# Kernel optimization log

Hardware: AMD Instinct MI355X
Metric: run time of the kernel (lower is better)

Reference implementation:

```python
import jax, jax.numpy as jnp
import numpy as np

N_NODES = 50000
N_EDGES = 800000
ATOM_DIM = 32
EDGE_DIM = 16
HIDDEN = 64
NUM_STEPS = 3
NUM_GRAPHS = 256
OUT_DIM = 1


def setup_inputs() -> dict:
    key = jax.random.key(0)
    ks = jax.random.split(key, 20)
    s = 0.05
    inp = {
        "x": jax.random.normal(ks[0], (N_NODES, ATOM_DIM), dtype=jnp.float32),
        "edge_index": jax.random.randint(ks[1], (2, N_EDGES), 0, N_NODES),
        "edge_attr": jax.random.normal(ks[2], (N_EDGES, EDGE_DIM), dtype=jnp.float32),
        "batch": jnp.sort(jax.random.randint(ks[3], (N_NODES,), 0, NUM_GRAPHS)),
        # atom embedding
        "W_embed": jax.random.normal(ks[4], (ATOM_DIM, HIDDEN)) * s,
        "b_embed": jnp.zeros((HIDDEN,)),
        # message MLP: Linear(2H+E, H) -> ReLU -> Linear(H, H)
        "W_m1": jax.random.normal(ks[5], (2 * HIDDEN + EDGE_DIM, HIDDEN)) * s,
        "b_m1": jnp.zeros((HIDDEN,)),
        "W_m2": jax.random.normal(ks[6], (HIDDEN, HIDDEN)) * s,
        "b_m2": jnp.zeros((HIDDEN,)),
        # GRUCell (torch layout: [3H, in] stacked r,z,n)
        "W_ih": jax.random.normal(ks[7], (3 * HIDDEN, HIDDEN)) * s,
        "b_ih": jnp.zeros((3 * HIDDEN,)),
        "W_hh": jax.random.normal(ks[8], (3 * HIDDEN, HIDDEN)) * s,
        "b_hh": jnp.zeros((3 * HIDDEN,)),
        # head: Linear(2H, H) -> ReLU -> Linear(H, out)
        "W_h1": jax.random.normal(ks[9], (2 * HIDDEN, HIDDEN)) * s,
        "b_h1": jnp.zeros((HIDDEN,)),
        "W_h2": jax.random.normal(ks[10], (HIDDEN, OUT_DIM)) * s,
        "b_h2": jnp.zeros((OUT_DIM,)),
    }
    return inp


def _gru_cell(inp, h, W_ih, b_ih, W_hh, b_hh):
    gi = inp @ W_ih.T + b_ih   # [N, 3H]
    gh = h @ W_hh.T + b_hh     # [N, 3H]
    i_r, i_z, i_n = jnp.split(gi, 3, axis=-1)
    h_r, h_z, h_n = jnp.split(gh, 3, axis=-1)
    r = jax.nn.sigmoid(i_r + h_r)
    z = jax.nn.sigmoid(i_z + h_z)
    n = jnp.tanh(i_n + r * h_n)
    return (1.0 - z) * n + z * h


def reference(x, edge_index, edge_attr, batch,
              W_embed, b_embed, W_m1, b_m1, W_m2, b_m2,
              W_ih, b_ih, W_hh, b_hh, W_h1, b_h1, W_h2, b_h2):
    h = x @ W_embed + b_embed                       # [N, H]
    src, dst = edge_index[0], edge_index[1]         # PyG: x_j = x[src], x_i = x[dst]
    for _ in range(NUM_STEPS):                      # tied weights
        m = jnp.concatenate([h[src], h[dst], edge_attr], axis=-1)  # [E, 2H+ED]
        m = jax.nn.relu(m @ W_m1 + b_m1) @ W_m2 + b_m2             # [E, H]
        agg = jax.ops.segment_sum(m, dst, num_segments=N_NODES)    # scatter-add
        h = _gru_cell(agg, h, W_ih, b_ih, W_hh, b_hh)
    g_sum = jax.ops.segment_sum(h, batch, num_segments=NUM_GRAPHS)  # [G, H]
    cnt = jax.ops.segment_sum(jnp.ones((N_NODES,), h.dtype), batch,
                              num_segments=NUM_GRAPHS)
    g_mean = g_sum / jnp.maximum(cnt, 1.0)[:, None]
    g = jnp.concatenate([g_sum, g_mean], axis=-1)   # [G, 2H]
    return jax.nn.relu(g @ W_h1 + b_h1) @ W_h2 + b_h2  # [G, out]
```

## Files before the change

kernel.cpp:

```cpp
#include <hip/hip_runtime.h>
#include <math.h>

#define NN 50000
#define NE 800000
#define AD 32
#define ED 16
#define HD 64
#define NG 256
#define NTILES (NE / 16)
#define EGRID 1280
#define EGRID_FB 1024
#define TPX (NTILES / 8)
#define GGRID 768
#define GTILES (NN / 16)
#define PGRID 782

typedef short bf16x8 __attribute__((ext_vector_type(8)));
typedef float f32x4  __attribute__((ext_vector_type(4)));
union U4B { uint4 u; bf16x8 v; };

__device__ __forceinline__ float blo(unsigned u){ return __uint_as_float(u << 16); }
__device__ __forceinline__ float bhi(unsigned u){ return __uint_as_float(u & 0xffff0000u); }
__device__ __forceinline__ unsigned short f2bf(float f){
  unsigned u = __float_as_uint(f);
  u += 0x7fffu + ((u >> 16) & 1u);
  return (unsigned short)(u >> 16);
}
__device__ __forceinline__ unsigned packbf2(float a, float b){
  return (unsigned)f2bf(a) | ((unsigned)f2bf(b) << 16);
}
__device__ __forceinline__ bf16x8 ldfrag_g(const unsigned* p){
  U4B x; x.u = *(const uint4*)p; return x.v;
}
__device__ __forceinline__ unsigned srp1(unsigned a, unsigned b, unsigned c){
  float lo = fmaxf(blo(a) + blo(b) + blo(c), 0.f);
  float hi = fmaxf(bhi(a) + bhi(b) + bhi(c), 0.f);
  return packbf2(lo, hi);
}
__device__ __forceinline__ bf16x8 srp4(uint4 a, uint4 b, uint4 c){
  U4B r;
  r.u.x = srp1(a.x, b.x, c.x);
  r.u.y = srp1(a.y, b.y, c.y);
  r.u.z = srp1(a.z, b.z, c.z);
  r.u.w = srp1(a.w, b.w, c.w);
  return r.v;
}

__global__ __launch_bounds__(256) void k_prep(const float* __restrict__ W1,
                                              const float* __restrict__ W2,
                                              const float* __restrict__ Wih,
                                              const float* __restrict__ Whh,
                                              const float* __restrict__ b1,
                                              unsigned short* __restrict__ W1Tp,
                                              unsigned short* __restrict__ W2Tp,
                                              unsigned short* __restrict__ Wgru,
                                              unsigned short* __restrict__ W1cTp)
{
  int idx = blockIdx.x * 256 + threadIdx.x;
  if (idx < 64 * 168){
    int n = idx / 168, k = idx % 168;
    W1Tp[idx] = (k < 144) ? f2bf(W1[k * 64 + n]) : (unsigned short)0;
    return;
  }
  idx -= 64 * 168;
  if (idx < 64 * 72){
    int n = idx / 72, k = idx % 72;
    W2Tp[idx] = (k < 64) ? f2bf(W2[k * 64 + n]) : (unsigned short)0;
    return;
  }
  idx -= 64 * 72;
  if (idx < 384 * 64){
    int j = idx & 7;
    int g = (idx >> 3) % 384;
    int blk = idx >> 3; blk /= 384;
    int q = blk & 3, ks = blk >> 2;
    int k = ks * 32 + q * 8 + j;
    float v = (g < 192) ? Wih[g * 64 + k] : Whh[(g - 192) * 64 + k];
    Wgru[idx] = f2bf(v);
    return;
  }
  idx -= 384 * 64;
  if (idx < 64 * 32){
    int n = idx / 32, k = idx % 32;
    float v = (k < 16) ? W1[(128 + k) * 64 + n] : (k == 16 ? b1[n] : 0.f);
    W1cTp[idx] = f2bf(v);
  }
}

__global__ __launch_bounds__(256) void k_hist(const int* __restrict__ eidx, int* __restrict__ deg)
{
  int e = blockIdx.x * 256 + threadIdx.x;
  if (e < NE) atomicAdd(&deg[eidx[NE + e]], 1);
}

__global__ __launch_bounds__(1024) void k_scan1(const int* __restrict__ deg,
                                                int* __restrict__ cur,
                                                int* __restrict__ bsum)
{
  __shared__ int s[1024];
  const int t = threadIdx.x;
  const int idx = blockIdx.x * 1024 + t;
  int v = (idx < NN) ? deg[idx] : 0;
  s[t] = v;
  __syncthreads();
  for (int d = 1; d < 1024; d <<= 1){
    int y = (t >= d) ? s[t - d] : 0;
    __syncthreads();
    s[t] += y;
    __syncthreads();
  }
  if (idx < NN) cur[idx] = s[t] - v;
  if (t == 1023) bsum[blockIdx.x] = s[1023];
}

__global__ __launch_bounds__(64) void k_scan2(const int* __restrict__ bsum,
                                              int* __restrict__ bpre)
{
  const int t = threadIdx.x;
  const int nb = (NN + 1023) / 1024;
  int v = (t < nb) ? bsum[t] : 0;
  int orig = v;
  #pragma unroll
  for (int off = 1; off < 64; off <<= 1){
    int u = __shfl_up(v, off);
    if (t >= off) v += u;
  }
  if (t < nb) bpre[t] = v - orig;
}

__global__ __launch_bounds__(1024) void k_scan3(int* __restrict__ cur,
                                                const int* __restrict__ bpre)
{
  const int idx = blockIdx.x * 1024 + threadIdx.x;
  if (idx < NN) cur[idx] += bpre[blockIdx.x];
}

__global__ __launch_bounds__(256) void k_scatter(const int* __restrict__ eidx,
                                                 const float* __restrict__ eattr,
                                                 int* __restrict__ cur,
                                                 int* __restrict__ src_s,
                                                 int* __restrict__ dst_s,
                                                 unsigned* __restrict__ eattr_bf)
{
  int e = blockIdx.x * 256 + threadIdx.x;
  if (e >= NE) return;
  int d = eidx[NE + e];
  int p = atomicAdd(&cur[d], 1);
  src_s[p] = eidx[e];
  dst_s[p] = d;
  const float* ea = eattr + (size_t)e * 16;
  float4 v0 = *(const float4*)(ea);
  float4 v1 = *(const float4*)(ea + 4);
  float4 v2 = *(const float4*)(ea + 8);
  float4 v3 = *(const float4*)(ea + 12);
  uint4 o0, o1;
  o0.x = packbf2(v0.x, v0.y); o0.y = packbf2(v0.z, v0.w);
  o0.z = packbf2(v1.x, v1.y); o0.w = packbf2(v1.z, v1.w);
  o1.x = packbf2(v2.x, v2.y); o1.y = packbf2(v2.z, v2.w);
  o1.z = packbf2(v3.x, v3.y); o1.w = packbf2(v3.z, v3.w);
  *(uint4*)(eattr_bf + (size_t)p * 8)     = o0;
  *(uint4*)(eattr_bf + (size_t)p * 8 + 4) = o1;
}

__global__ __launch_bounds__(256) void k_eprep(const unsigned* __restrict__ eattr_bf,
                                               const unsigned* __restrict__ W1cTp32,
                                               unsigned* __restrict__ E1)
{
  const int t = threadIdx.x, lane = t & 63, wv = t >> 6;
  const int m = lane & 15, q = lane >> 4;
  bf16x8 wf[4];
  #pragma unroll
  for (int tl = 0; tl < 4; ++tl)
    wf[tl] = ldfrag_g(W1cTp32 + (tl * 16 + m) * 16 + q * 4);

  for (int wt = blockIdx.x * 4 + wv; wt < NTILES; wt += 1024 * 4){
    const int base = wt * 16;
    U4B x;
    if (q < 2)      x.u = *(const uint4*)(eattr_bf + (size_t)(base + m) * 8 + q * 4);
    else if (q == 2) x.u = make_uint4(0x3F80u, 0, 0, 0);
    else             x.u = make_uint4(0, 0, 0, 0);
    bf16x8 a = x.v;
    f32x4 c[4];
    #pragma unroll
    for (int tl = 0; tl < 4; ++tl) c[tl] = f32x4{0.f,0.f,0.f,0.f};
    #pragma unroll
    for (int tl = 0; tl < 4; ++tl)
      c[tl] = __builtin_amdgcn_mfma_f32_16x16x32_bf16(a, wf[tl], c[tl], 0, 0, 0);
    #pragma unroll
    for (int tl = 0; tl < 4; ++tl){
      #pragma unroll
      for (int rr = 0; rr < 4; ++rr){
        float v = c[tl][rr];
        float pp = __shfl_xor(v, 1);
        if (!(m & 1))
          E1[(size_t)(base + q * 4 + rr) * 32 + (tl * 16 + m) / 2] = packbf2(v, pp);
      }
    }
  }
}

__global__ __launch_bounds__(256, 4) void k_pre(const unsigned* __restrict__ h_bf,
                                                const unsigned short* __restrict__ W1Tp,
                                                unsigned* __restrict__ C12)
{
  const int t = threadIdx.x, lane = t & 63, wv = t >> 6;
  const int m = lane & 15, q = lane >> 4;
  bf16x8 wa[4][2], wb[4][2];
  #pragma unroll
  for (int tl = 0; tl < 4; ++tl)
    #pragma unroll
    for (int ks = 0; ks < 2; ++ks){
      wa[tl][ks] = ldfrag_g((const unsigned*)(W1Tp + (tl * 16 + m) * 168 + ks * 32 + q * 8));
      wb[tl][ks] = ldfrag_g((const unsigned*)(W1Tp + (tl * 16 + m) * 168 + 64 + ks * 32 + q * 8));
    }
  for (int wt = blockIdx.x * 4 + wv; wt < GTILES; wt += PGRID * 4){
    const int n0 = wt * 16;
    bf16x8 aH[2];
    #pragma unroll
    for (int ks = 0; ks < 2; ++ks)
      aH[ks] = ldfrag_g(h_bf + (size_t)(n0 + m) * 32 + ks * 16 + q * 4);
    f32x4 ca[4], cb[4];
    #pragma unroll
    for (int tl = 0; tl < 4; ++tl){ ca[tl] = f32x4{0.f,0.f,0.f,0.f}; cb[tl] = ca[tl]; }
    #pragma unroll
    for (int ks = 0; ks < 2; ++ks)
      #pragma unroll
      for (int tl = 0; tl < 4; ++tl){
        ca[tl] = __builtin_amdgcn_mfma_f32_16x16x32_bf16(aH[ks], wa[tl][ks], ca[tl], 0, 0, 0);
        cb[tl] = __builtin_amdgcn_mfma_f32_16x16x32_bf16(aH[ks], wb[tl][ks], cb[tl], 0, 0, 0);
      }
    #pragma unroll
    for (int tl = 0; tl < 4; ++tl){
      #pragma unroll
      for (int rr = 0; rr < 4; ++rr){
        const int node = n0 + q * 4 + rr;
        float va = ca[tl][rr], vb = cb[tl][rr];
        float pa = __shfl_xor(va, 1), pb = __shfl_xor(vb, 1);
        if (!(m & 1)){
          C12[(size_t)node * 64 + (tl * 16 + m) / 2]      = packbf2(va, pa);
          C12[(size_t)node * 64 + 32 + (tl * 16 + m) / 2] = packbf2(vb, pb);
        }
      }
    }
  }
}

__global__ __launch_bounds__(256) void k_embed(const float* __restrict__ x,
                                               const float* __restrict__ We,
                                               const float* __restrict__ be,
                                               float* __restrict__ h,
                                               unsigned* __restrict__ h_bf)
{
  const int t = threadIdx.x;
  const int j = t & 63, nd = t >> 6;
  const int node = blockIdx.x * 4 + nd;
  const float* xr = x + (size_t)node * AD;
  float acc = be[j];
  #pragma unroll 8
  for (int k = 0; k < AD; ++k)
    acc += xr[k] * We[k * HD + j];
  h[(size_t)node * HD + j] = acc;
  float p = __shfl_down(acc, 1);
  if (!(j & 1)) h_bf[(size_t)node * 32 + (j >> 1)] = packbf2(acc, p);
}

__global__ __launch_bounds__(256, 4) void k_edge(const unsigned* __restrict__ C12,
                                                 const unsigned* __restrict__ E1,
                                                 const int* __restrict__ src_s,
                                                 const int* __restrict__ dst_s,
                                                 const unsigned* __restrict__ W2Tp32,
                                                 const float* __restrict__ b2,
                                                 float* __restrict__ agg)
{
  const int t = threadIdx.x;
  const int lane = t & 63, wv = t >> 6;
  const int m = lane & 15, q = lane >> 4;

  bf16x8 w2f[4][2];
  #pragma unroll
  for (int tl = 0; tl < 4; ++tl)
    #pragma unroll
    for (int ks = 0; ks < 2; ++ks)
      w2f[tl][ks] = ldfrag_g(W2Tp32 + (tl * 16 + m) * 36 + ks * 16 + q * 4);

  float b2v[4];
  #pragma unroll
  for (int tl = 0; tl < 4; ++tl) b2v[tl] = b2[tl * 16 + m];

  const int xcd = blockIdx.x & 7, bi = blockIdx.x >> 3;
  const int wend = (xcd + 1) * TPX;
  const int wstep = (EGRID / 8) * 4;
  int wt = xcd * TPX + bi * 4 + wv;

  int scur = src_s[wt * 16 + m];
  int dcur = dst_s[wt * 16 + m];

  while (wt < wend){
    const int wn = wt + wstep;
    const bool hasn = (wn < wend);
    int sn = 0, dn = 0;
    if (hasn){ sn = src_s[wn * 16 + m]; dn = dst_s[wn * 16 + m]; }

    const unsigned* c1p = C12 + (size_t)scur * 64;
    const unsigned* c2p = C12 + (size_t)dcur * 64 + 32;
    const unsigned* e1p = E1 + (size_t)(wt * 16 + m) * 32;
    uint4 c1a = *(const uint4*)(c1p + q * 4);
    uint4 c1b = *(const uint4*)(c1p + 16 + q * 4);
    uint4 c2a = *(const uint4*)(c2p + q * 4);
    uint4 c2b = *(const uint4*)(c2p + 16 + q * 4);
    uint4 e1a = *(const uint4*)(e1p + q * 4);
    uint4 e1b = *(const uint4*)(e1p + 16 + q * 4);

    bf16x8 af0 = srp4(c1a, c2a, e1a);
    bf16x8 af1 = srp4(c1b, c2b, e1b);

    f32x4 o0 = {0.f,0.f,0.f,0.f}, o1 = o0, o2 = o0, o3 = o0;
    o0 = __builtin_amdgcn_mfma_f32_16x16x32_bf16(af0, w2f[0][0], o0, 0, 0, 0);
    o1 = __builtin_amdgcn_mfma_f32_16x16x32_bf16(af0, w2f[1][0], o1, 0, 0, 0);
    o2 = __builtin_amdgcn_mfma_f32_16x16x32_bf16(af0, w2f[2][0], o2, 0, 0, 0);
    o3 = __builtin_amdgcn_mfma_f32_16x16x32_bf16(af0, w2f[3][0], o3, 0, 0, 0);
    o0 = __builtin_amdgcn_mfma_f32_16x16x32_bf16(af1, w2f[0][1], o0, 0, 0, 0);
    o1 = __builtin_amdgcn_mfma_f32_16x16x32_bf16(af1, w2f[1][1], o1, 0, 0, 0);
    o2 = __builtin_amdgcn_mfma_f32_16x16x32_bf16(af1, w2f[2][1], o2, 0, 0, 0);
    o3 = __builtin_amdgcn_mfma_f32_16x16x32_bf16(af1, w2f[3][1], o3, 0, 0, 0);

    int prev = __shfl_up(dcur, 1);
    bool isStart = (m == 0) || (dcur != prev);
    unsigned long long bal = __ballot(isStart);
    unsigned bs = (unsigned)bal & 0xFFFFu;
    int nr = __popc(bs);
    unsigned rem = bs & (bs - 1);
    int lo = 0;
    for (int r = 0; r < nr; ++r){
      int hi = rem ? (__ffs(rem) - 1) : 16;
      rem &= rem - 1;
      float s0 = 0.f, s1 = 0.f, s2 = 0.f, s3 = 0.f;
      #pragma unroll
      for (int rr = 0; rr < 4; ++rr){
        int row = q * 4 + rr;
        bool in = (row >= lo) && (row < hi);
        s0 += in ? o0[rr] : 0.f;
        s1 += in ? o1[rr] : 0.f;
        s2 += in ? o2[rr] : 0.f;
        s3 += in ? o3[rr] : 0.f;
      }
      s0 += __shfl_xor(s0, 16); s0 += __shfl_xor(s0, 32);
      s1 += __shfl_xor(s1, 16); s1 += __shfl_xor(s1, 32);
      s2 += __shfl_xor(s2, 16); s2 += __shfl_xor(s2, 32);
      s3 += __shfl_xor(s3, 16); s3 += __shfl_xor(s3, 32);
      int d = __shfl(dcur, lo);
      float cntf = (float)(hi - lo);
      if (q == 0){
        float v0 = s0 + cntf * b2v[0];
        float v1 = s1 + cntf * b2v[1];
        float v2 = s2 + cntf * b2v[2];
        float v3 = s3 + cntf * b2v[3];
        float* dp = &agg[(size_t)d * HD + m];
        if (r == 0 || r == nr - 1){
          atomicAdd(dp +  0, v0); atomicAdd(dp + 16, v1);
          atomicAdd(dp + 32, v2); atomicAdd(dp + 48, v3);
        } else {
          dp[ 0] = v0; dp[16] = v1; dp[32] = v2; dp[48] = v3;
        }
      }
      lo = hi;
    }

    wt = wn; scur = sn; dcur = dn;
  }
}

__global__ __launch_bounds__(256, 3) void k_edge_fb(const unsigned* __restrict__ h_bf,
                                                    const int* __restrict__ src_s,
                                                    const int* __restrict__ dst_s,
                                                    const unsigned* __restrict__ eattr_bf,
                                                    const unsigned short* __restrict__ W1Tp,
                                                    const float* __restrict__ b1,
                                                    const unsigned* __restrict__ W2Tp32,
                                                    const float* __restrict__ b2,
                                                    float* __restrict__ agg)
{
  __shared__ __align__(16) unsigned short sW1T[64 * 168];
  __shared__ __align__(16) unsigned short sHid[4][16 * 72];

  const int t = threadIdx.x;
  {
    const uint4* srcp = (const uint4*)W1Tp;
    uint4* dstp = (uint4*)sW1T;
    for (int i = t; i < 64 * 168 * 2 / 16; i += 256) dstp[i] = srcp[i];
  }
  __syncthreads();

  const int lane = t & 63, wv = t >> 6;
  const int m = lane & 15, q = lane >> 4;

  bf16x8 w2f[4][2];
  #pragma unroll
  for (int tl = 0; tl < 4; ++tl)
    #pragma unroll
    for (int ks = 0; ks < 2; ++ks)
      w2f[tl][ks] = ldfrag_g(W2Tp32 + (tl * 16 + m) * 36 + ks * 16 + q * 4);

  float b1v[4], b2v[4];
  #pragma unroll
  for (int tl = 0; tl < 4; ++tl){ b1v[tl] = b1[tl * 16 + m]; b2v[tl] = b2[tl * 16 + m]; }

  unsigned short* sHidW = sHid[wv];

  const int xcd = blockIdx.x & 7, bi = blockIdx.x >> 3;
  const int wend = (xcd + 1) * TPX;
  const int wstep = (EGRID_FB / 8) * 4;
  int wt = xcd * TPX + bi * 4 + wv;

  int scur = src_s[wt * 16 + m];
  int dcur = dst_s[wt * 16 + m];
  bf16x8 afc[5];
  {
    const unsigned* hs = h_bf + (size_t)scur * 32;
    const unsigned* hd = h_bf + (size_t)dcur * 32;
    afc[0] = ldfrag_g(hs + q * 4);
    afc[1] = ldfrag_g(hs + 16 + q * 4);
    afc[2] = ldfrag_g(hd + q * 4);
    afc[3] = ldfrag_g(hd + 16 + q * 4);
    if (q < 2) afc[4] = ldfrag_g(eattr_bf + (size_t)(wt * 16 + m) * 8 + q * 4);
    else { U4B x; x.u = make_uint4(0,0,0,0); afc[4] = x.v; }
  }

  while (wt < wend){
    const int wn = wt + wstep;
    const bool hasn = (wn < wend);
    int sn = 0, dn = 0;
    if (hasn){ sn = src_s[wn * 16 + m]; dn = dst_s[wn * 16 + m]; }

    f32x4 a0 = {0.f,0.f,0.f,0.f}, a1 = a0, a2 = a0, a3 = a0;
    #pragma unroll
    for (int ks = 0; ks < 5; ++ks){
      bf16x8 bb0 = *(const bf16x8*)&sW1T[( 0 + m) * 168 + ks * 32 + q * 8];
      bf16x8 bb1 = *(const bf16x8*)&sW1T[(16 + m) * 168 + ks * 32 + q * 8];
      bf16x8 bb2 = *(const bf16x8*)&sW1T[(32 + m) * 168 + ks * 32 + q * 8];
      bf16x8 bb3 = *(const bf16x8*)&sW1T[(48 + m) * 168 + ks * 32 + q * 8];
      a0 = __builtin_amdgcn_mfma_f32_16x16x32_bf16(afc[ks], bb0, a0, 0, 0, 0);
      a1 = __builtin_amdgcn_mfma_f32_16x16x32_bf16(afc[ks], bb1, a1, 0, 0, 0);
      a2 = __builtin_amdgcn_mfma_f32_16x16x32_bf16(afc[ks], bb2, a2, 0, 0, 0);
      a3 = __builtin_amdgcn_mfma_f32_16x16x32_bf16(afc[ks], bb3, a3, 0, 0, 0);
    }
    {
      f32x4 accs[4] = {a0, a1, a2, a3};
      #pragma unroll
      for (int tl = 0; tl < 4; ++tl)
        #pragma unroll
        for (int r = 0; r < 4; ++r)
          sHidW[(q * 4 + r) * 72 + tl * 16 + m] = f2bf(fmaxf(accs[tl][r] + b1v[tl], 0.f));
    }

    bf16x8 afn[5];
    if (hasn){
      const unsigned* hs = h_bf + (size_t)sn * 32;
      const unsigned* hd = h_bf + (size_t)dn * 32;
      afn[0] = ldfrag_g(hs + q * 4);
      afn[1] = ldfrag_g(hs + 16 + q * 4);
      afn[2] = ldfrag_g(hd + q * 4);
      afn[3] = ldfrag_g(hd + 16 + q * 4);
      if (q < 2) afn[4] = ldfrag_g(eattr_bf + (size_t)(wn * 16 + m) * 8 + q * 4);
      else { U4B x; x.u = make_uint4(0,0,0,0); afn[4] = x.v; }
    }

    f32x4 o0 = {0.f,0.f,0.f,0.f}, o1 = o0, o2 = o0, o3 = o0;
    #pragma unroll
    for (int ks = 0; ks < 2; ++ks){
      bf16x8 av = *(const bf16x8*)&sHidW[m * 72 + ks * 32 + q * 8];
      o0 = __builtin_amdgcn_mfma_f32_16x16x32_bf16(av, w2f[0][ks], o0, 0, 0, 0);
      o1 = __builtin_amdgcn_mfma_f32_16x16x32_bf16(av, w2f[1][ks], o1, 0, 0, 0);
      o2 = __builtin_amdgcn_mfma_f32_16x16x32_bf16(av, w2f[2][ks], o2, 0, 0, 0);
      o3 = __builtin_amdgcn_mfma_f32_16x16x32_bf16(av, w2f[3][ks], o3, 0, 0, 0);
    }

    int prev = __shfl_up(dcur, 1);
    bool isStart = (m == 0) || (dcur != prev);
    unsigned long long bal = __ballot(isStart);
    unsigned bs = (unsigned)bal & 0xFFFFu;
    int nr = __popc(bs);
    unsigned rem = bs & (bs - 1);
    int lo = 0;
    for (int r = 0; r < nr; ++r){
      int hi = rem ? (__ffs(rem) - 1) : 16;
      rem &= rem - 1;
      float s0 = 0.f, s1 = 0.f, s2 = 0.f, s3 = 0.f;
      #pragma unroll
      for (int rr = 0; rr < 4; ++rr){
        int row = q * 4 + rr;
        bool in = (row >= lo) && (row < hi);
        s0 += in ? o0[rr] : 0.f;
        s1 += in ? o1[rr] : 0.f;
        s2 += in ? o2[rr] : 0.f;
        s3 += in ? o3[rr] : 0.f;
      }
      s0 += __shfl_xor(s0, 16); s0 += __shfl_xor(s0, 32);
      s1 += __shfl_xor(s1, 16); s1 += __shfl_xor(s1, 32);
      s2 += __shfl_xor(s2, 16); s2 += __shfl_xor(s2, 32);
      s3 += __shfl_xor(s3, 16); s3 += __shfl_xor(s3, 32);
      int d = __shfl(dcur, lo);
      float cntf = (float)(hi - lo);
      if (q == 0){
        float v0 = s0 + cntf * b2v[0];
        float v1 = s1 + cntf * b2v[1];
        float v2 = s2 + cntf * b2v[2];
        float v3 = s3 + cntf * b2v[3];
        float* dp = &agg[(size_t)d * HD + m];
        if (r == 0 || r == nr - 1){
          atomicAdd(dp +  0, v0); atomicAdd(dp + 16, v1);
          atomicAdd(dp + 32, v2); atomicAdd(dp + 48, v3);
        } else {
          dp[ 0] = v0; dp[16] = v1; dp[32] = v2; dp[48] = v3;
        }
      }
      lo = hi;
    }

    wt = wn; scur = sn; dcur = dn;
    #pragma unroll
    for (int i = 0; i < 5; ++i) afc[i] = afn[i];
  }
}

__global__ __launch_bounds__(256) void k_gru(const float* __restrict__ agg,
                                             float* __restrict__ h,
                                             unsigned* __restrict__ h_bf,
                                             const unsigned short* __restrict__ Wgru,
                                             const float* __restrict__ bih,
                                             const float* __restrict__ bhh)
{
  __shared__ __align__(16) unsigned short sWg[384 * 64];

  const int t = threadIdx.x;
  {
    const uint4* srcp = (const uint4*)Wgru;
    uint4* dstp = (uint4*)sWg;
    for (int i = t; i < 384 * 64 * 2 / 16; i += 256) dstp[i] = srcp[i];
  }
  __syncthreads();

  const int lane = t & 63, wv = t >> 6;
  const int m = lane & 15, q = lane >> 4;

  float bi_r[4], bi_z[4], bi_n[4], bh_r[4], bh_z[4], bh_n[4];
  #pragma unroll
  for (int tl = 0; tl < 4; ++tl){
    bi_r[tl] = bih[tl * 16 + m];  bi_z[tl] = bih[64 + tl * 16 + m];  bi_n[tl] = bih[128 + tl * 16 + m];
    bh_r[tl] = bhh[tl * 16 + m];  bh_z[tl] = bhh[64 + tl * 16 + m];  bh_n[tl] = bhh[128 + tl * 16 + m];
  }

  for (int wt = blockIdx.x * 4 + wv; wt < GTILES; wt += GGRID * 4){
    const int n0 = wt * 16;

    bf16x8 aA[2], aH[2];
    #pragma unroll
    for (int ks = 0; ks < 2; ++ks){
      const float* ap = agg + (size_t)(n0 + m) * 64 + ks * 32 + q * 8;
      float4 v0 = *(const float4*)ap;
      float4 v1 = *(const float4*)(ap + 4);
      U4B x;
      x.u.x = packbf2(v0.x, v0.y); x.u.y = packbf2(v0.z, v0.w);
      x.u.z = packbf2(v1.x, v1.y); x.u.w = packbf2(v1.z, v1.w);
      aA[ks] = x.v;
      aH[ks] = ldfrag_g(h_bf + (size_t)(n0 + m) * 32 + ks * 16 + q * 4);
    }

    f32x4 ci[12], ch[12];
    #pragma unroll
    for (int tl = 0; tl < 12; ++tl){ ci[tl] = f32x4{0.f,0.f,0.f,0.f}; ch[tl] = ci[tl]; }
    #pragma unroll
    for (int ks = 0; ks < 2; ++ks){
      #pragma unroll
      for (int tl = 0; tl < 12; ++tl){
        bf16x8 bi = *(const bf16x8*)&sWg[((ks * 4 + q) * 384 + tl * 16 + m) * 8];
        ci[tl] = __builtin_amdgcn_mfma_f32_16x16x32_bf16(aA[ks], bi, ci[tl], 0, 0, 0);
        bf16x8 bh = *(const bf16x8*)&sWg[((ks * 4 + q) * 384 + 192 + tl * 16 + m) * 8];
        ch[tl] = __builtin_amdgcn_mfma_f32_16x16x32_bf16(aH[ks], bh, ch[tl], 0, 0, 0);
      }
    }

    #pragma unroll
    for (int tl = 0; tl < 4; ++tl){
      #pragma unroll
      for (int rr = 0; rr < 4; ++rr){
        const int node = n0 + q * 4 + rr;
        float ir = ci[tl][rr]     + bi_r[tl], hr = ch[tl][rr]     + bh_r[tl];
        float iz = ci[4 + tl][rr] + bi_z[tl], hz = ch[4 + tl][rr] + bh_z[tl];
        float in_ = ci[8 + tl][rr] + bi_n[tl], hn = ch[8 + tl][rr] + bh_n[tl];
        float rg = 1.f / (1.f + __expf(-(ir + hr)));
        float zg = 1.f / (1.f + __expf(-(iz + hz)));
        float ng = tanhf(in_ + rg * hn);
        float hold = h[(size_t)node * HD + tl * 16 + m];
        float hnew = (1.f - zg) * ng + zg * hold;
        h[(size_t)node * HD + tl * 16 + m] = hnew;
        float pp = __shfl_xor(hnew, 1);
        if (!(m & 1))
          h_bf[(size_t)node * 32 + tl * 8 + (m >> 1)] = packbf2(hnew, pp);
      }
    }
  }
}

__global__ __launch_bounds__(256) void k_pool(const float* __restrict__ h,
                                              const int* __restrict__ batch,
                                              float* __restrict__ gsum,
                                              float* __restrict__ cnt)
{
  const int t = threadIdx.x;
  const int j = t & 63, r = t >> 6;
  const int n0 = blockIdx.x * 64 + r * 16;
  float acc = 0.f, c = 0.f;
  int cur = -1;
  for (int i = 0; i < 16; ++i){
    int n = n0 + i;
    if (n >= NN) break;
    int g = batch[n];
    if (g != cur){
      if (cur >= 0){
        atomicAdd(&gsum[cur * HD + j], acc);
        if (j == 0) atomicAdd(&cnt[cur], c);
      }
      cur = g; acc = 0.f; c = 0.f;
    }
    acc += h[(size_t)n * HD + j];
    c += 1.f;
  }
  if (cur >= 0){
    atomicAdd(&gsum[cur * HD + j], acc);
    if (j == 0) atomicAdd(&cnt[cur], c);
  }
}

__global__ __launch_bounds__(64) void k_head(const float* __restrict__ gsum,
                                             const float* __restrict__ cnt,
                                             const float* __restrict__ W1,
                                             const float* __restrict__ b1,
                                             const float* __restrict__ W2,
                                             const float* __restrict__ b2,
                                             float* __restrict__ out)
{
  __shared__ float gv[128];
  const int g = blockIdx.x, j = threadIdx.x;
  float s = gsum[g * HD + j];
  float c = cnt[g];
  gv[j] = s;
  gv[64 + j] = s / fmaxf(c, 1.f);
  __syncthreads();
  float acc = b1[j];
  #pragma unroll 8
  for (int k = 0; k < 128; ++k)
    acc += gv[k] * W1[k * HD + j];
  acc = fmaxf(acc, 0.f);
  float v = acc * W2[j];
  #pragma unroll
  for (int off = 32; off; off >>= 1) v += __shfl_down(v, off, 64);
  if (j == 0) out[g] = v + b2[0];
}

extern "C" void kernel_launch(void* const* d_in, const int* in_sizes, int n_in,
                              void* d_out, int out_size, void* d_ws, size_t ws_size,
                              hipStream_t stream)
{
  (void)in_sizes; (void)n_in; (void)out_size;
  const float* x     = (const float*)d_in[0];
  const int*   eidx  = (const int*)d_in[1];
  const float* eattr = (const float*)d_in[2];
  const int*   batch = (const int*)d_in[3];
  const float* We    = (const float*)d_in[4];
  const float* be    = (const float*)d_in[5];
  const float* Wm1   = (const float*)d_in[6];
  const float* bm1   = (const float*)d_in[7];
  const float* Wm2   = (const float*)d_in[8];
  const float* bm2   = (const float*)d_in[9];
  const float* Wih   = (const float*)d_in[10];
  const float* bih   = (const float*)d_in[11];
  const float* Whh   = (const float*)d_in[12];
  const float* bhh   = (const float*)d_in[13];
  const float* Wh1   = (const float*)d_in[14];
  const float* bh1   = (const float*)d_in[15];
  const float* Wh2   = (const float*)d_in[16];
  const float* bh2   = (const float*)d_in[17];

  char* w0 = (char*)d_ws;
  char* w = w0;
  float* h     = (float*)w;                      w += (size_t)NN * HD * 4;
  unsigned* h_bf = (unsigned*)w;                 w += (size_t)NN * 32 * 4;
  float* agg   = (float*)w;                      w += (size_t)NN * HD * 4;
  int*   deg   = (int*)w;                        w += (size_t)NN * 4;
  int*   cur   = (int*)w;                        w += (size_t)NN * 4;
  int*   src_s = (int*)w;                        w += (size_t)NE * 4;
  int*   dst_s = (int*)w;                        w += (size_t)NE * 4;
  unsigned* eattr_bf = (unsigned*)w;             w += (size_t)NE * 8 * 4;
  int*   bsum  = (int*)w;                        w += 64 * 4;
  int*   bpre  = (int*)w;                        w += 64 * 4;
  unsigned short* W1Tp = (unsigned short*)w;     w += 64 * 168 * 2;
  unsigned short* W2Tp = (unsigned short*)w;     w += 64 * 72 * 2;
  unsigned short* Wgru = (unsigned short*)w;     w += 384 * 64 * 2;
  unsigned short* W1cTp = (unsigned short*)w;    w += 64 * 32 * 2;
  float* gsum  = (float*)w;                      w += (size_t)NG * HD * 4;
  float* cnt   = (float*)w;                      w += (size_t)NG * 4;
  unsigned* C12 = (unsigned*)w;                  w += (size_t)NN * 64 * 4;
  unsigned* E1  = (unsigned*)w;                  w += (size_t)NE * 32 * 4;
  const bool full = ((size_t)(w - w0) <= ws_size);

  const int nscanb = (NN + 1023) / 1024;

  k_prep<<<164, 256, 0, stream>>>(Wm1, Wm2, Wih, Whh, bm1, W1Tp, W2Tp, Wgru, W1cTp);
  hipMemsetAsync(deg, 0, (size_t)NN * 4, stream);
  k_hist<<<(NE + 255) / 256, 256, 0, stream>>>(eidx, deg);
  k_scan1<<<nscanb, 1024, 0, stream>>>(deg, cur, bsum);
  k_scan2<<<1, 64, 0, stream>>>(bsum, bpre);
  k_scan3<<<nscanb, 1024, 0, stream>>>(cur, bpre);
  k_scatter<<<(NE + 255) / 256, 256, 0, stream>>>(eidx, eattr, cur, src_s, dst_s, eattr_bf);
  if (full)
    k_eprep<<<1024, 256, 0, stream>>>(eattr_bf, (const unsigned*)W1cTp, E1);

  k_embed<<<NN / 4, 256, 0, stream>>>(x, We, be, h, h_bf);
  for (int s = 0; s < 3; ++s){
    hipMemsetAsync(agg, 0, (size_t)NN * HD * 4, stream);
    if (full){
      k_pre<<<PGRID, 256, 0, stream>>>(h_bf, W1Tp, C12);
      k_edge<<<EGRID, 256, 0, stream>>>(C12, E1, src_s, dst_s,
                                        (const unsigned*)W2Tp, bm2, agg);
    } else {
      k_edge_fb<<<EGRID_FB, 256, 0, stream>>>(h_bf, src_s, dst_s, eattr_bf, W1Tp, bm1,
                                              (const unsigned*)W2Tp, bm2, agg);
    }
    k_gru<<<GGRID, 256, 0, stream>>>(agg, h, h_bf, Wgru, bih, bhh);
  }
  hipMemsetAsync(gsum, 0, (size_t)(NG * HD + NG) * 4, stream);
  k_pool<<<(NN + 63) / 64, 256, 0, stream>>>(h, batch, gsum, cnt);
  k_head<<<NG, 64, 0, stream>>>(gsum, cnt, Wh1, bh1, Wh2, bh2, (float*)d_out);
}
```

Baseline: 578.6 us.

## Pack sorted edge records, compute E1 in original order, fuse agg zeroing

Scatter now writes a packed int4 (src,dst,edge id) per sorted edge instead of separate src/dst arrays plus a bf16 edge-attr copy. The edge-attr projection E1 is computed directly from fp32 eattr in original order, and the edge kernel gathers it by original edge id. The per-step agg memset is folded into the embed and GRU kernels. This trades setup traffic and memset launches for a random gather of E1 rows in every message step; the workspace-size fallback path is removed.

```diff
diff --git a/kernel.cpp b/kernel.cpp
--- a/kernel.cpp
+++ b/kernel.cpp
@@ -9,7 +9,6 @@
 #define NG 256
 #define NTILES (NE / 16)
 #define EGRID 1280
-#define EGRID_FB 1024
 #define TPX (NTILES / 8)
 #define GGRID 768
 #define GTILES (NN / 16)
@@ -136,35 +135,20 @@
 }
 
 __global__ __launch_bounds__(256) void k_scatter(const int* __restrict__ eidx,
-                                                 const float* __restrict__ eattr,
                                                  int* __restrict__ cur,
-                                                 int* __restrict__ src_s,
-                                                 int* __restrict__ dst_s,
-                                                 unsigned* __restrict__ eattr_bf)
+                                                 int4* __restrict__ sde)
 {
   int e = blockIdx.x * 256 + threadIdx.x;
   if (e >= NE) return;
+  int s = eidx[e];
   int d = eidx[NE + e];
   int p = atomicAdd(&cur[d], 1);
-  src_s[p] = eidx[e];
-  dst_s[p] = d;
-  const float* ea = eattr + (size_t)e * 16;
-  float4 v0 = *(const float4*)(ea);
-  float4 v1 = *(const float4*)(ea + 4);
-  float4 v2 = *(const float4*)(ea + 8);
-  float4 v3 = *(const float4*)(ea + 12);
-  uint4 o0, o1;
-  o0.x = packbf2(v0.x, v0.y); o0.y = packbf2(v0.z, v0.w);
-  o0.z = packbf2(v1.x, v1.y); o0.w = packbf2(v1.z, v1.w);
-  o1.x = packbf2(v2.x, v2.y); o1.y = packbf2(v2.z, v2.w);
-  o1.z = packbf2(v3.x, v3.y); o1.w = packbf2(v3.z, v3.w);
-  *(uint4*)(eattr_bf + (size_t)p * 8)     = o0;
-  *(uint4*)(eattr_bf + (size_t)p * 8 + 4) = o1;
-}
-
-__global__ __launch_bounds__(256) void k_eprep(const unsigned* __restrict__ eattr_bf,
+  sde[p] = make_int4(s, d, e, 0);
+}
+
+__global__ __launch_bounds__(256) void k_eprep(const float* __restrict__ eattr,
                                                const unsigned* __restrict__ W1cTp32,
-                                               unsigned* __restrict__ E1)
+                                               unsigned* __restrict__ E1o)
 {
   const int t = threadIdx.x, lane = t & 63, wv = t >> 6;
   const int m = lane & 15, q = lane >> 4;
@@ -176,9 +160,14 @@
   for (int wt = blockIdx.x * 4 + wv; wt < NTILES; wt += 1024 * 4){
     const int base = wt * 16;
     U4B x;
-    if (q < 2)      x.u = *(const uint4*)(eattr_bf + (size_t)(base + m) * 8 + q * 4);
-    else if (q == 2) x.u = make_uint4(0x3F80u, 0, 0, 0);
-    else             x.u = make_uint4(0, 0, 0, 0);
+    if (q < 2){
+      const float* ea = eattr + (size_t)(base + m) * 16 + q * 8;
+      float4 v0 = *(const float4*)(ea);
+      float4 v1 = *(const float4*)(ea + 4);
+      x.u.x = packbf2(v0.x, v0.y); x.u.y = packbf2(v0.z, v0.w);
+      x.u.z = packbf2(v1.x, v1.y); x.u.w = packbf2(v1.z, v1.w);
+    } else if (q == 2) x.u = make_uint4(0x3F80u, 0, 0, 0);
+    else               x.u = make_uint4(0, 0, 0, 0);
     bf16x8 a = x.v;
     f32x4 c[4];
     #pragma unroll
@@ -193,7 +182,7 @@
         float v = c[tl][rr];
         float pp = __shfl_xor(v, 1);
         if (!(m & 1))
-          E1[(size_t)(base + q * 4 + rr) * 32 + (tl * 16 + m) / 2] = packbf2(v, pp);
+          E1o[(size_t)(base + q * 4 + rr) * 32 + (tl * 16 + m) / 2] = packbf2(v, pp);
       }
     }
   }
@@ -249,7 +238,8 @@
                                                const float* __restrict__ We,
                                                const float* __restrict__ be,
                                                float* __restrict__ h,
-                                               unsigned* __restrict__ h_bf)
+                                               unsigned* __restrict__ h_bf,
+                                               float* __restrict__ agg)
 {
   const int t = threadIdx.x;
   const int j = t & 63, nd = t >> 6;
@@ -260,14 +250,14 @@
   for (int k = 0; k < AD; ++k)
     acc += xr[k] * We[k * HD + j];
   h[(size_t)node * HD + j] = acc;
+  agg[(size_t)node * HD + j] = 0.f;
   float p = __shfl_down(acc, 1);
   if (!(j & 1)) h_bf[(size_t)node * 32 + (j >> 1)] = packbf2(acc, p);
 }
 
 __global__ __launch_bounds__(256, 4) void k_edge(const unsigned* __restrict__ C12,
-                                                 const unsigned* __restrict__ E1,
-                                                 const int* __restrict__ src_s,
-                                                 const int* __restrict__ dst_s,
+                                                 const unsigned* __restrict__ E1o,
+                                                 const int4* __restrict__ sde,
                                                  const unsigned* __restrict__ W2Tp32,
                                                  const float* __restrict__ b2,
                                                  float* __restrict__ agg)
@@ -292,18 +282,19 @@
   const int wstep = (EGRID / 8) * 4;
   int wt = xcd * TPX + bi * 4 + wv;
 
-  int scur = src_s[wt * 16 + m];
-  int dcur = dst_s[wt * 16 + m];
+  int4 cursde = sde[wt * 16 + m];
 
   while (wt < wend){
     const int wn = wt + wstep;
     const bool hasn = (wn < wend);
-    int sn = 0, dn = 0;
-    if (hasn){ sn = src_s[wn * 16 + m]; dn = dst_s[wn * 16 + m]; }
+    int4 nsde = make_int4(0, 0, 0, 0);
+    if (hasn) nsde = sde[wn * 16 + m];
+
+    const int scur = cursde.x, dcur = cursde.y, ecur = cursde.z;
 
     const unsigned* c1p = C12 + (size_t)scur * 64;
     const unsigned* c2p = C12 + (size_t)dcur * 64 + 32;
-    const unsigned* e1p = E1 + (size_t)(wt * 16 + m) * 32;
+    const unsigned* e1p = E1o + (size_t)ecur * 32;
     uint4 c1a = *(const uint4*)(c1p + q * 4);
     uint4 c1b = *(const uint4*)(c1p + 16 + q * 4);
     uint4 c2a = *(const uint4*)(c2p + q * 4);
@@ -366,164 +357,11 @@
       lo = hi;
     }
 
-    wt = wn; scur = sn; dcur = dn;
-  }
-}
-
-__global__ __launch_bounds__(256, 3) void k_edge_fb(const unsigned* __restrict__ h_bf,
-                                                    const int* __restrict__ src_s,
-                                                    const int* __restrict__ dst_s,
-                                                    const unsigned* __restrict__ eattr_bf,
-                                                    const unsigned short* __restrict__ W1Tp,
-                                                    const float* __restrict__ b1,
-                                                    const unsigned* __restrict__ W2Tp32,
-                                                    const float* __restrict__ b2,
-                                                    float* __restrict__ agg)
-{
-  __shared__ __align__(16) unsigned short sW1T[64 * 168];
-  __shared__ __align__(16) unsigned short sHid[4][16 * 72];
-
-  const int t = threadIdx.x;
-  {
-    const uint4* srcp = (const uint4*)W1Tp;
-    uint4* dstp = (uint4*)sW1T;
-    for (int i = t; i < 64 * 168 * 2 / 16; i += 256) dstp[i] = srcp[i];
-  }
-  __syncthreads();
-
-  const int lane = t & 63, wv = t >> 6;
-  const int m = lane & 15, q = lane >> 4;
-
-  bf16x8 w2f[4][2];
-  #pragma unroll
-  for (int tl = 0; tl < 4; ++tl)
-    #pragma unroll
-    for (int ks = 0; ks < 2; ++ks)
-      w2f[tl][ks] = ldfrag_g(W2Tp32 + (tl * 16 + m) * 36 + ks * 16 + q * 4);
-
-  float b1v[4], b2v[4];
-  #pragma unroll
-  for (int tl = 0; tl < 4; ++tl){ b1v[tl] = b1[tl * 16 + m]; b2v[tl] = b2[tl * 16 + m]; }
-
-  unsigned short* sHidW = sHid[wv];
-
-  const int xcd = blockIdx.x & 7, bi = blockIdx.x >> 3;
-  const int wend = (xcd + 1) * TPX;
-  const int wstep = (EGRID_FB / 8) * 4;
-  int wt = xcd * TPX + bi * 4 + wv;
-
-  int scur = src_s[wt * 16 + m];
-  int dcur = dst_s[wt * 16 + m];
-  bf16x8 afc[5];
-  {
-    const unsigned* hs = h_bf + (size_t)scur * 32;
-    const unsigned* hd = h_bf + (size_t)dcur * 32;
-    afc[0] = ldfrag_g(hs + q * 4);
-    afc[1] = ldfrag_g(hs + 16 + q * 4);
-    afc[2] = ldfrag_g(hd + q * 4);
-    afc[3] = ldfrag_g(hd + 16 + q * 4);
-    if (q < 2) afc[4] = ldfrag_g(eattr_bf + (size_t)(wt * 16 + m) * 8 + q * 4);
-    else { U4B x; x.u = make_uint4(0,0,0,0); afc[4] = x.v; }
-  }
-
-  while (wt < wend){
-    const int wn = wt + wstep;
-    const bool hasn = (wn < wend);
-    int sn = 0, dn = 0;
-    if (hasn){ sn = src_s[wn * 16 + m]; dn = dst_s[wn * 16 + m]; }
-
-    f32x4 a0 = {0.f,0.f,0.f,0.f}, a1 = a0, a2 = a0, a3 = a0;
-    #pragma unroll
-    for (int ks = 0; ks < 5; ++ks){
-      bf16x8 bb0 = *(const bf16x8*)&sW1T[( 0 + m) * 168 + ks * 32 + q * 8];
-      bf16x8 bb1 = *(const bf16x8*)&sW1T[(16 + m) * 168 + ks * 32 + q * 8];
-      bf16x8 bb2 = *(const bf16x8*)&sW1T[(32 + m) * 168 + ks * 32 + q * 8];
-      bf16x8 bb3 = *(const bf16x8*)&sW1T[(48 + m) * 168 + ks * 32 + q * 8];
-      a0 = __builtin_amdgcn_mfma_f32_16x16x32_bf16(afc[ks], bb0, a0, 0, 0, 0);
-      a1 = __builtin_amdgcn_mfma_f32_16x16x32_bf16(afc[ks], bb1, a1, 0, 0, 0);
-      a2 = __builtin_amdgcn_mfma_f32_16x16x32_bf16(afc[ks], bb2, a2, 0, 0, 0);
-      a3 = __builtin_amdgcn_mfma_f32_16x16x32_bf16(afc[ks], bb3, a3, 0, 0, 0);
-    }
-    {
-      f32x4 accs[4] = {a0, a1, a2, a3};
-      #pragma unroll
-      for (int tl = 0; tl < 4; ++tl)
-        #pragma unroll
-        for (int r = 0; r < 4; ++r)
-          sHidW[(q * 4 + r) * 72 + tl * 16 + m] = f2bf(fmaxf(accs[tl][r] + b1v[tl], 0.f));
-    }
-
-    bf16x8 afn[5];
-    if (hasn){
-      const unsigned* hs = h_bf + (size_t)sn * 32;
-      const unsigned* hd = h_bf + (size_t)dn * 32;
-      afn[0] = ldfrag_g(hs + q * 4);
-      afn[1] = ldfrag_g(hs + 16 + q * 4);
-      afn[2] = ldfrag_g(hd + q * 4);
-      afn[3] = ldfrag_g(hd + 16 + q * 4);
-      if (q < 2) afn[4] = ldfrag_g(eattr_bf + (size_t)(wn * 16 + m) * 8 + q * 4);
-      else { U4B x; x.u = make_uint4(0,0,0,0); afn[4] = x.v; }
-    }
-
-    f32x4 o0 = {0.f,0.f,0.f,0.f}, o1 = o0, o2 = o0, o3 = o0;
-    #pragma unroll
-    for (int ks = 0; ks < 2; ++ks){
-      bf16x8 av = *(const bf16x8*)&sHidW[m * 72 + ks * 32 + q * 8];
-      o0 = __builtin_amdgcn_mfma_f32_16x16x32_bf16(av, w2f[0][ks], o0, 0, 0, 0);
-      o1 = __builtin_amdgcn_mfma_f32_16x16x32_bf16(av, w2f[1][ks], o1, 0, 0, 0);
-      o2 = __builtin_amdgcn_mfma_f32_16x16x32_bf16(av, w2f[2][ks], o2, 0, 0, 0);
-      o3 = __builtin_amdgcn_mfma_f32_16x16x32_bf16(av, w2f[3][ks], o3, 0, 0, 0);
-    }
-
-    int prev = __shfl_up(dcur, 1);
-    bool isStart = (m == 0) || (dcur != prev);
-    unsigned long long bal = __ballot(isStart);
-    unsigned bs = (unsigned)bal & 0xFFFFu;
-    int nr = __popc(bs);
-    unsigned rem = bs & (bs - 1);
-    int lo = 0;
-    for (int r = 0; r < nr; ++r){
-      int hi = rem ? (__ffs(rem) - 1) : 16;
-      rem &= rem - 1;
-      float s0 = 0.f, s1 = 0.f, s2 = 0.f, s3 = 0.f;
-      #pragma unroll
-      for (int rr = 0; rr < 4; ++rr){
-        int row = q * 4 + rr;
-        bool in = (row >= lo) && (row < hi);
-        s0 += in ? o0[rr] : 0.f;
-        s1 += in ? o1[rr] : 0.f;
-        s2 += in ? o2[rr] : 0.f;
-        s3 += in ? o3[rr] : 0.f;
-      }
-      s0 += __shfl_xor(s0, 16); s0 += __shfl_xor(s0, 32);
-      s1 += __shfl_xor(s1, 16); s1 += __shfl_xor(s1, 32);
-      s2 += __shfl_xor(s2, 16); s2 += __shfl_xor(s2, 32);
-      s3 += __shfl_xor(s3, 16); s3 += __shfl_xor(s3, 32);
-      int d = __shfl(dcur, lo);
-      float cntf = (float)(hi - lo);
-      if (q == 0){
-        float v0 = s0 + cntf * b2v[0];
-        float v1 = s1 + cntf * b2v[1];
-        float v2 = s2 + cntf * b2v[2];
-        float v3 = s3 + cntf * b2v[3];
-        float* dp = &agg[(size_t)d * HD + m];
-        if (r == 0 || r == nr - 1){
-          atomicAdd(dp +  0, v0); atomicAdd(dp + 16, v1);
-          atomicAdd(dp + 32, v2); atomicAdd(dp + 48, v3);
-        } else {
-          dp[ 0] = v0; dp[16] = v1; dp[32] = v2; dp[48] = v3;
-        }
-      }
-      lo = hi;
-    }
-
-    wt = wn; scur = sn; dcur = dn;
-    #pragma unroll
-    for (int i = 0; i < 5; ++i) afc[i] = afn[i];
-  }
-}
-
-__global__ __launch_bounds__(256) void k_gru(const float* __restrict__ agg,
+    wt = wn; cursde = nsde;
+  }
+}
+
+__global__ __launch_bounds__(256) void k_gru(float* __restrict__ agg,
                                              float* __restrict__ h,
                                              unsigned* __restrict__ h_bf,
                                              const unsigned short* __restrict__ Wgru,
@@ -594,6 +432,7 @@
         float hold = h[(size_t)node * HD + tl * 16 + m];
         float hnew = (1.f - zg) * ng + zg * hold;
         h[(size_t)node * HD + tl * 16 + m] = hnew;
+        agg[(size_t)node * HD + tl * 16 + m] = 0.f;
         float pp = __shfl_xor(hnew, 1);
         if (!(m & 1))
           h_bf[(size_t)node * 32 + tl * 8 + (m >> 1)] = packbf2(hnew, pp);
@@ -662,7 +501,7 @@
                               void* d_out, int out_size, void* d_ws, size_t ws_size,
                               hipStream_t stream)
 {
-  (void)in_sizes; (void)n_in; (void)out_size;
+  (void)in_sizes; (void)n_in; (void)out_size; (void)ws_size;
   const float* x     = (const float*)d_in[0];
   const int*   eidx  = (const int*)d_in[1];
   const float* eattr = (const float*)d_in[2];
@@ -682,16 +521,13 @@
   const float* Wh2   = (const float*)d_in[16];
   const float* bh2   = (const float*)d_in[17];
 
-  char* w0 = (char*)d_ws;
-  char* w = w0;
+  char* w = (char*)d_ws;
   float* h     = (float*)w;                      w += (size_t)NN * HD * 4;
   unsigned* h_bf = (unsigned*)w;                 w += (size_t)NN * 32 * 4;
   float* agg   = (float*)w;                      w += (size_t)NN * HD * 4;
   int*   deg   = (int*)w;                        w += (size_t)NN * 4;
   int*   cur   = (int*)w;                        w += (size_t)NN * 4;
-  int*   src_s = (int*)w;                        w += (size_t)NE * 4;
-  int*   dst_s = (int*)w;                        w += (size_t)NE * 4;
-  unsigned* eattr_bf = (unsigned*)w;             w += (size_t)NE * 8 * 4;
+  int4*  sde   = (int4*)w;                       w += (size_t)NE * 16;
   int*   bsum  = (int*)w;                        w += 64 * 4;
   int*   bpre  = (int*)w;                        w += 64 * 4;
   unsigned short* W1Tp = (unsigned short*)w;     w += 64 * 168 * 2;
@@ -701,8 +537,7 @@
   float* gsum  = (float*)w;                      w += (size_t)NG * HD * 4;
   float* cnt   = (float*)w;                      w += (size_t)NG * 4;
   unsigned* C12 = (unsigned*)w;                  w += (size_t)NN * 64 * 4;
-  unsigned* E1  = (unsigned*)w;                  w += (size_t)NE * 32 * 4;
-  const bool full = ((size_t)(w - w0) <= ws_size);
+  unsigned* E1o = (unsigned*)w;                  w += (size_t)NE * 32 * 4;
 
   const int nscanb = (NN + 1023) / 1024;
 
@@ -712,21 +547,13 @@
   k_scan1<<<nscanb, 1024, 0, stream>>>(deg, cur, bsum);
   k_scan2<<<1, 64, 0, stream>>>(bsum, bpre);
   k_scan3<<<nscanb, 1024, 0, stream>>>(cur, bpre);
-  k_scatter<<<(NE + 255) / 256, 256, 0, stream>>>(eidx, eattr, cur, src_s, dst_s, eattr_bf);
-  if (full)
-    k_eprep<<<1024, 256, 0, stream>>>(eattr_bf, (const unsigned*)W1cTp, E1);
-
-  k_embed<<<NN / 4, 256, 0, stream>>>(x, We, be, h, h_bf);
+  k_scatter<<<(NE + 255) / 256, 256, 0, stream>>>(eidx, cur, sde);
+  k_eprep<<<1024, 256, 0, stream>>>(eattr, (const unsigned*)W1cTp, E1o);
+
+  k_embed<<<NN / 4, 256, 0, stream>>>(x, We, be, h, h_bf, agg);
   for (int s = 0; s < 3; ++s){
-    hipMemsetAsync(agg, 0, (size_t)NN * HD * 4, stream);
-    if (full){
-      k_pre<<<PGRID, 256, 0, stream>>>(h_bf, W1Tp, C12);
-      k_edge<<<EGRID, 256, 0, stream>>>(C12, E1, src_s, dst_s,
-                                        (const unsigned*)W2Tp, bm2, agg);
-    } else {
-      k_edge_fb<<<EGRID_FB, 256, 0, stream>>>(h_bf, src_s, dst_s, eattr_bf, W1Tp, bm1,
-                                              (const unsigned*)W2Tp, bm2, agg);
-    }
+    k_pre<<<PGRID, 256, 0, stream>>>(h_bf, W1Tp, C12);
+    k_edge<<<EGRID, 256, 0, stream>>>(C12, E1o, sde, (const unsigned*)W2Tp, bm2, agg);
     k_gru<<<GGRID, 256, 0, stream>>>(agg, h, h_bf, Wgru, bih, bhh);
   }
   hipMemsetAsync(gsum, 0, (size_t)(NG * HD + NG) * 4, stream);
```

Measured after the change: 594.6 us. 1.03x slower.
